# Optimization experiments

Measured on AMD Instinct MI355X. Metric: run time of the kernel, lower is better.

The kernel has to match this reference:

```python
import jax, jax.numpy as jnp
import numpy as np

# Model constants (match init_kwargs / input_specs)
D_MODEL = 64; N_HEADS = 4; D_HEAD = D_MODEL // N_HEADS
N_LAYERS = 2; D_FF = 256
N_GRAPHS = 256; NODES_PER = 64; N_NODES = N_GRAPHS * NODES_PER
DEG = 8; N_EDGES = N_NODES * DEG
VOCAB = 32; N_CLASS = 10


def setup_inputs() -> dict:
    rng = np.random.default_rng(0)
    # node labels
    x = jnp.asarray(rng.integers(0, VOCAB, N_NODES), dtype=jnp.int32)
    # sparse edge_index: each node receives DEG messages from random nodes in its own graph
    base = np.repeat(np.arange(N_NODES), DEG)
    nbr = (base // NODES_PER) * NODES_PER + rng.integers(0, NODES_PER, N_NODES * DEG)
    edge_index = jnp.asarray(np.stack([nbr, base]), dtype=jnp.int32)  # [2, E] (src, dst)
    # complete_edge_index: all (src, dst) pairs within each graph
    local = np.arange(NODES_PER); goff = np.arange(N_GRAPHS) * NODES_PER
    ii = np.repeat(local, NODES_PER); jj = np.tile(local, NODES_PER)
    c_src = (goff[:, None] + ii[None, :]).reshape(-1)
    c_dst = (goff[:, None] + jj[None, :]).reshape(-1)
    complete_edge_index = jnp.asarray(np.stack([c_src, c_dst]), dtype=jnp.int32)  # [2, 1048576]
    batch = jnp.asarray(np.repeat(np.arange(N_GRAPHS), NODES_PER), dtype=jnp.int32)

    key = jax.random.key(0)
    ks = jax.random.split(key, 12)
    s = 1.0 / np.sqrt(D_MODEL)
    W = lambda k, shape, sc: jax.random.normal(k, shape, jnp.float32) * sc
    return {
        'x': x, 'edge_index': edge_index, 'complete_edge_index': complete_edge_index, 'batch': batch,
        'emb': W(ks[0], (VOCAB, D_MODEL), 0.1),
        'Wg_self': W(ks[1], (N_LAYERS, D_MODEL, D_MODEL), s),
        'Wg_nbr': W(ks[2], (N_LAYERS, D_MODEL, D_MODEL), s),
        'Wq': W(ks[3], (N_LAYERS, D_MODEL, D_MODEL), s),
        'Wk': W(ks[4], (N_LAYERS, D_MODEL, D_MODEL), s),
        'Wv': W(ks[5], (N_LAYERS, D_MODEL, D_MODEL), s),
        'Wo': W(ks[6], (N_LAYERS, D_MODEL, D_MODEL), s),
        'bo': jnp.zeros((N_LAYERS, D_MODEL), jnp.float32),
        'ln1_g': jnp.ones((N_LAYERS, D_MODEL), jnp.float32),
        'ln1_b': jnp.zeros((N_LAYERS, D_MODEL), jnp.float32),
        'ff_W1': W(ks[7], (N_LAYERS, D_MODEL, D_FF), s),
        'ff_b1': jnp.zeros((N_LAYERS, D_FF), jnp.float32),
        'ff_W2': W(ks[8], (N_LAYERS, D_FF, D_MODEL), 1.0 / np.sqrt(D_FF)),
        'ff_b2': jnp.zeros((N_LAYERS, D_MODEL), jnp.float32),
        'ln2_g': jnp.ones((N_LAYERS, D_MODEL), jnp.float32),
        'ln2_b': jnp.zeros((N_LAYERS, D_MODEL), jnp.float32),
        'c_W1': W(ks[9], (D_MODEL, D_MODEL), s),
        'c_b1': jnp.zeros((D_MODEL,), jnp.float32),
        'c_W2': W(ks[10], (D_MODEL, N_CLASS), s),
        'c_b2': jnp.zeros((N_CLASS,), jnp.float32),
    }


def _layernorm(h, g, b):
    m = jnp.mean(h, -1, keepdims=True)
    v = jnp.var(h, -1, keepdims=True)
    return (h - m) * jax.lax.rsqrt(v + 1e-5) * g + b


def _forward(x, edge_index, complete_edge_index, batch, emb, Wg_self, Wg_nbr, Wq, Wk, Wv, Wo, bo,
             ln1_g, ln1_b, ff_W1, ff_b1, ff_W2, ff_b2, ln2_g, ln2_b, c_W1, c_b1, c_W2, c_b2):
    e_src, e_dst = edge_index[0], edge_index[1]
    c_src, c_dst = complete_edge_index[0], complete_edge_index[1]
    h = emb[x]  # [N, d] embedding lookup
    inv_sqrt = 1.0 / np.sqrt(D_HEAD)
    for i in range(N_LAYERS):
        # --- structure extractor: one GNN message-passing step over sparse edge_index ---
        agg = jax.ops.segment_sum((h @ Wg_nbr[i])[e_src], e_dst, num_segments=N_NODES)
        struct = h + jax.nn.relu(h @ Wg_self[i] + agg)
        # --- multi-head attention over complete_edge_index (full attention within graph) ---
        q = (struct @ Wq[i]).reshape(N_NODES, N_HEADS, D_HEAD)
        k = (struct @ Wk[i]).reshape(N_NODES, N_HEADS, D_HEAD)
        v = (h @ Wv[i]).reshape(N_NODES, N_HEADS, D_HEAD)
        scores = jnp.einsum('ehd,ehd->eh', q[c_dst], k[c_src]) * inv_sqrt  # [Ec, H]
        m = jax.ops.segment_max(scores, c_dst, num_segments=N_NODES)
        ex = jnp.exp(scores - m[c_dst])
        den = jax.ops.segment_sum(ex, c_dst, num_segments=N_NODES)
        alpha = ex / den[c_dst]  # segment softmax per destination node
        attn = jax.ops.segment_sum(alpha[:, :, None] * v[c_src], c_dst, num_segments=N_NODES)
        out = attn.reshape(N_NODES, D_MODEL) @ Wo[i] + bo[i]
        h = _layernorm(h + out, ln1_g[i], ln1_b[i])
        # --- feed-forward ---
        f = jax.nn.relu(h @ ff_W1[i] + ff_b1[i]) @ ff_W2[i] + ff_b2[i]
        h = _layernorm(h + f, ln2_g[i], ln2_b[i])
    # --- global mean pooling per graph + classifier ---
    counts = jax.ops.segment_sum(jnp.ones((N_NODES,), jnp.float32), batch, num_segments=N_GRAPHS)
    pooled = jax.ops.segment_sum(h, batch, num_segments=N_GRAPHS) / counts[:, None]
    return jax.nn.relu(pooled @ c_W1 + c_b1) @ c_W2 + c_b2  # [B, num_class]


def reference(x, edge_index, complete_edge_index, batch, emb, Wg_self, Wg_nbr, Wq, Wk, Wv, Wo, bo,
              ln1_g, ln1_b, ff_W1, ff_b1, ff_W2, ff_b2, ln2_g, ln2_b, c_W1, c_b1, c_W2, c_b2):
    return _forward(x, edge_index, complete_edge_index, batch, emb, Wg_self, Wg_nbr, Wq, Wk, Wv, Wo,
                    bo, ln1_g, ln1_b, ff_W1, ff_b1, ff_W2, ff_b2, ln2_g, ln2_b, c_W1, c_b1, c_W2, c_b2)
```

## Files before the change

kernel.cpp:

```cpp
#include <hip/hip_runtime.h>

#define NG 256
#define NPG 64
#define DM 64
#define DFF 256
#define NL 2
#define DEG 8
#define NCLS 10
#define S68 68
#define S132 132

#define HB0 0
#define AB0 4352
#define BB0 8704
#define QB0 13056
#define WS0 17408
#define F10 26112
#define POOLW 34560

typedef __attribute__((ext_vector_type(4))) float f32x4;
typedef __attribute__((ext_vector_type(4))) unsigned int u32x4;
typedef __attribute__((ext_vector_type(8))) __bf16 bf16x8;

__device__ __forceinline__ unsigned int packsplit(float x) {
    union { float f; unsigned int u; } a; a.f = x;
    const unsigned int t = a.u;
    const unsigned int hi = (t + 0x7FFFu + ((t >> 16) & 1u)) >> 16;
    union { unsigned int u; float f; } hf; hf.u = hi << 16;
    union { float f; unsigned int u; } b; b.f = x - hf.f;
    const unsigned int tl = b.u;
    const unsigned int lo = (tl + 0x7FFFu + ((tl >> 16) & 1u)) & 0xFFFF0000u;
    return hi | lo;
}
__device__ __forceinline__ float unpackf(unsigned int u) {
    union { unsigned int u; float f; } h, l;
    h.u = u << 16;
    l.u = u & 0xFFFF0000u;
    return h.f + l.f;
}

__device__ __forceinline__ void extract(u32x4 p0, u32x4 p1, u32x4& hi, u32x4& lo) {
    hi[0] = (p0[0] & 0xFFFFu) | (p0[1] << 16);
    hi[1] = (p0[2] & 0xFFFFu) | (p0[3] << 16);
    hi[2] = (p1[0] & 0xFFFFu) | (p1[1] << 16);
    hi[3] = (p1[2] & 0xFFFFu) | (p1[3] << 16);
    lo[0] = (p0[0] >> 16) | (p0[1] & 0xFFFF0000u);
    lo[1] = (p0[2] >> 16) | (p0[3] & 0xFFFF0000u);
    lo[2] = (p1[0] >> 16) | (p1[1] & 0xFFFF0000u);
    lo[3] = (p1[2] >> 16) | (p1[3] & 0xFFFF0000u);
}

__device__ __forceinline__ f32x4 mfma16(u32x4 a, u32x4 b, f32x4 c) {
    return __builtin_amdgcn_mfma_f32_16x16x32_bf16(
        __builtin_bit_cast(bf16x8, a), __builtin_bit_cast(bf16x8, b), c, 0, 0, 0);
}

__device__ __forceinline__ f32x4 mmchunk(const unsigned int* Ap, const unsigned int* Bp,
                                         f32x4 acc) {
    const u32x4 a0 = *(const u32x4*)Ap, a1 = *(const u32x4*)(Ap + 4);
    const u32x4 b0 = *(const u32x4*)Bp, b1 = *(const u32x4*)(Bp + 4);
    u32x4 ah, al, bh, bl;
    extract(a0, a1, ah, al);
    extract(b0, b1, bh, bl);
    acc = mfma16(ah, bh, acc);
    acc = mfma16(ah, bl, acc);
    acc = mfma16(al, bh, acc);
    return acc;
}

__device__ __forceinline__ f32x4 mm64(const unsigned int* Apk, const unsigned int* Wst,
                                      int wr, int wc, int l) {
    const int arow = (wr << 4) + (l & 15);
    const int bcol = (wc << 4) + (l & 15);
    const int kg = (l >> 4) << 3;
    f32x4 acc = {0.f, 0.f, 0.f, 0.f};
    acc = mmchunk(Apk + arow * S68 + kg,      Wst + bcol * S68 + kg,      acc);
    acc = mmchunk(Apk + arow * S68 + kg + 32, Wst + bcol * S68 + kg + 32, acc);
    return acc;
}

__device__ __forceinline__ void dwrite_f32(float* dst, f32x4 acc, int wr, int wc, int l) {
    const int col = (wc << 4) + (l & 15);
    const int r0 = (wr << 4) + ((l >> 4) << 2);
#pragma unroll
    for (int r = 0; r < 4; ++r) dst[(r0 + r) * S68 + col] = acc[r];
}

__device__ __forceinline__ void stageW(const float* W, unsigned int* ws, int tid) {
    const int k = tid >> 4, c4 = (tid & 15) << 2;
    const f32x4 w = *(const f32x4*)(W + k * DM + c4);
#pragma unroll
    for (int i = 0; i < 4; ++i) ws[(c4 + i) * S68 + k] = packsplit(w[i]);
}

__device__ __forceinline__ void layernorm(const float* src, unsigned int* dst,
                                          const float* gp, const float* bp, int n, int jg) {
    const f32x4 v = *(const f32x4*)(src + n * S68 + jg);
    float s1 = v[0] + v[1] + v[2] + v[3];
    float s2 = v[0]*v[0] + v[1]*v[1] + v[2]*v[2] + v[3]*v[3];
    s1 += __shfl_xor(s1, 1); s1 += __shfl_xor(s1, 2);
    s1 += __shfl_xor(s1, 4); s1 += __shfl_xor(s1, 8);
    s2 += __shfl_xor(s2, 1); s2 += __shfl_xor(s2, 2);
    s2 += __shfl_xor(s2, 4); s2 += __shfl_xor(s2, 8);
    const float mean = s1 * 0.015625f;
    const float var  = s2 * 0.015625f - mean * mean;
    const float rstd = rsqrtf(var + 1e-5f);
    const f32x4 gm = *(const f32x4*)(gp + jg);
    const f32x4 bt = *(const f32x4*)(bp + jg);
    u32x4 p;
#pragma unroll
    for (int j = 0; j < 4; ++j) p[j] = packsplit((v[j] - mean) * rstd * gm[j] + bt[j]);
    *(u32x4*)(dst + n * S68 + jg) = p;
}

extern "C" __global__ __launch_bounds__(1024)
void gt_main(const int* __restrict__ x, const int* __restrict__ e_src,
             const float* __restrict__ emb, const float* __restrict__ Wgs,
             const float* __restrict__ Wgn, const float* __restrict__ Wq,
             const float* __restrict__ Wk, const float* __restrict__ Wv,
             const float* __restrict__ Wo, const float* __restrict__ bo,
             const float* __restrict__ l1g, const float* __restrict__ l1b,
             const float* __restrict__ fW1, const float* __restrict__ fb1,
             const float* __restrict__ fW2, const float* __restrict__ fb2,
             const float* __restrict__ l2g, const float* __restrict__ l2b,
             const float* __restrict__ cW1, const float* __restrict__ cb1,
             const float* __restrict__ cW2, const float* __restrict__ cb2,
             float* __restrict__ out)
{
    __shared__ unsigned int pool[POOLW];
    unsigned int* Hb  = pool + HB0;
    unsigned int* Abu = pool + AB0;  float* Abf = (float*)Abu;
    unsigned int* Bbu = pool + BB0;  float* Bbf = (float*)Bbu;
    unsigned int* Qbu = pool + QB0;  float* Qbf = (float*)Qbu;
    unsigned int* WsA = pool + WS0;
    unsigned int* WsB = pool + WS0 + 4352;
    unsigned int* Ws  = pool + WS0;
    unsigned int* F1  = pool + F10;

    const int g = blockIdx.x, tid = threadIdx.x;
    const int w = tid >> 6, l = tid & 63;
    const int wr = w >> 2, wc = w & 3;
    const int n = tid >> 4, c = tid & 15, jg = c << 2;

    {
        const int lbl = x[g * NPG + n];
        const f32x4 e = *(const f32x4*)(emb + lbl * DM + jg);
        u32x4 p;
#pragma unroll
        for (int j = 0; j < 4; ++j) p[j] = packsplit(e[j]);
        *(u32x4*)(Hb + n * S68 + jg) = p;
    }
    __syncthreads();

    for (int lay = 0; lay < NL; ++lay) {
        const int o64 = lay * DM * DM;

        stageW(Wgn + o64, WsA, tid); __syncthreads();
        { f32x4 acc = mm64(Hb, WsA, wr, wc, l); dwrite_f32(Abf, acc, wr, wc, l); }
        __syncthreads();

        {
            f32x4 s = {0.f, 0.f, 0.f, 0.f};
            const int* es = e_src + (g * NPG + n) * DEG;
#pragma unroll
            for (int k = 0; k < DEG; ++k) {
                const int sr = es[k] - g * NPG;
                const f32x4 v4 = *(const f32x4*)(Abf + sr * S68 + jg);
                s[0] += v4[0]; s[1] += v4[1]; s[2] += v4[2]; s[3] += v4[3];
            }
            *(f32x4*)(Bbf + n * S68 + jg) = s;
        }
        __syncthreads();

        stageW(Wgs + o64, WsB, tid); __syncthreads();
        {
            f32x4 acc = mm64(Hb, WsB, wr, wc, l);
            const int col = (wc << 4) + (l & 15), r0 = (wr << 4) + ((l >> 4) << 2);
#pragma unroll
            for (int r = 0; r < 4; ++r) {
                const int row = r0 + r;
                const float v = fmaxf(acc[r] + Bbf[row * S68 + col], 0.f)
                                + unpackf(Hb[row * S68 + col]);
                Abu[row * S68 + col] = packsplit(v);
            }
        }
        __syncthreads();

        stageW(Wk + o64, WsA, tid); __syncthreads();
        { f32x4 acc = mm64(Abu, WsA, wr, wc, l); dwrite_f32(Bbf, acc, wr, wc, l); }
        __syncthreads();

        stageW(Wq + o64, WsB, tid); __syncthreads();
        { f32x4 acc = mm64(Abu, WsB, wr, wc, l); dwrite_f32(Qbf, acc, wr, wc, l); }
        __syncthreads();

        stageW(Wv + o64, WsA, tid); __syncthreads();
        { f32x4 acc = mm64(Hb, WsA, wr, wc, l); dwrite_f32(Abf, acc, wr, wc, l); }
        __syncthreads();

        {
            const f32x4 q4 = *(const f32x4*)(Qbf + n * S68 + jg);
            float o0 = 0.f, o1 = 0.f, o2 = 0.f, o3 = 0.f, m = -1e30f, ls = 0.f;
            for (int sr = 0; sr < NPG; ++sr) {
                const f32x4 k4 = *(const f32x4*)(Bbf + sr * S68 + jg);
                float s = q4[0]*k4[0] + q4[1]*k4[1] + q4[2]*k4[2] + q4[3]*k4[3];
                s += __shfl_xor(s, 1);
                s += __shfl_xor(s, 2);
                s *= 0.25f;
                const float mn  = fmaxf(m, s);
                const float fac = __expf(m - mn), wg = __expf(s - mn);
                ls = ls * fac + wg;
                const f32x4 v4 = *(const f32x4*)(Abf + sr * S68 + jg);
                o0 = o0 * fac + wg * v4[0]; o1 = o1 * fac + wg * v4[1];
                o2 = o2 * fac + wg * v4[2]; o3 = o3 * fac + wg * v4[3];
                m = mn;
            }
            const float il = 1.f / ls;
            u32x4 p;
            p[0] = packsplit(o0 * il); p[1] = packsplit(o1 * il);
            p[2] = packsplit(o2 * il); p[3] = packsplit(o3 * il);
            *(u32x4*)(Qbu + n * S68 + jg) = p;
        }
        __syncthreads();

        stageW(Wo + o64, WsB, tid); __syncthreads();
        {
            f32x4 acc = mm64(Qbu, WsB, wr, wc, l);
            const int col = (wc << 4) + (l & 15), r0 = (wr << 4) + ((l >> 4) << 2);
            const float bb = bo[lay * DM + col];
#pragma unroll
            for (int r = 0; r < 4; ++r) {
                const int row = r0 + r;
                Abf[row * S68 + col] = acc[r] + bb + unpackf(Hb[row * S68 + col]);
            }
        }
        __syncthreads();

        layernorm(Abf, Hb, l1g + lay * DM, l1b + lay * DM, n, jg);
        __syncthreads();

        f32x4 f2 = {0.f, 0.f, 0.f, 0.f};
        for (int hf = 0; hf < 2; ++hf) {
            {
                const int k = tid >> 4, c8 = (tid & 15) << 3;
                const float* src = fW1 + lay * DM * DFF + k * DFF + hf * 128 + c8;
                const f32x4 w0 = *(const f32x4*)src, w1 = *(const f32x4*)(src + 4);
#pragma unroll
                for (int i = 0; i < 4; ++i) Ws[(c8 + i) * S68 + k]     = packsplit(w0[i]);
#pragma unroll
                for (int i = 0; i < 4; ++i) Ws[(c8 + 4 + i) * S68 + k] = packsplit(w1[i]);
            }
            __syncthreads();
            {
                const int kg = (l >> 4) << 3, arow = (wr << 4) + (l & 15);
                const int r0 = (wr << 4) + ((l >> 4) << 2);
#pragma unroll
                for (int t = 0; t < 2; ++t) {
                    const int tc = ((wc + 4 * t) << 4) + (l & 15);
                    f32x4 acc = {0.f, 0.f, 0.f, 0.f};
                    acc = mmchunk(Hb + arow * S68 + kg,      Ws + tc * S68 + kg,      acc);
                    acc = mmchunk(Hb + arow * S68 + kg + 32, Ws + tc * S68 + kg + 32, acc);
                    const float b1 = fb1[lay * DFF + hf * 128 + tc];
#pragma unroll
                    for (int r = 0; r < 4; ++r)
                        F1[(r0 + r) * S132 + tc] = packsplit(fmaxf(acc[r] + b1, 0.f));
                }
            }
            __syncthreads();
            {
                const int kk = tid >> 3, c8 = (tid & 7) << 3;
                const float* src = fW2 + lay * DFF * DM + (hf * 128 + kk) * DM + c8;
                const f32x4 w0 = *(const f32x4*)src, w1 = *(const f32x4*)(src + 4);
#pragma unroll
                for (int i = 0; i < 4; ++i) Ws[(c8 + i) * S132 + kk]     = packsplit(w0[i]);
#pragma unroll
                for (int i = 0; i < 4; ++i) Ws[(c8 + 4 + i) * S132 + kk] = packsplit(w1[i]);
            }
            __syncthreads();
            {
                const int kg = (l >> 4) << 3;
                const int arow = (wr << 4) + (l & 15), bcol = (wc << 4) + (l & 15);
#pragma unroll
                for (int ch = 0; ch < 4; ++ch)
                    f2 = mmchunk(F1 + arow * S132 + kg + 32 * ch,
                                 Ws + bcol * S132 + kg + 32 * ch, f2);
            }
            __syncthreads();
        }
        {
            const int col = (wc << 4) + (l & 15), r0 = (wr << 4) + ((l >> 4) << 2);
            const float bb = fb2[lay * DM + col];
#pragma unroll
            for (int r = 0; r < 4; ++r) {
                const int row = r0 + r;
                Abf[row * S68 + col] = f2[r] + bb + unpackf(Hb[row * S68 + col]);
            }
        }
        __syncthreads();

        layernorm(Abf, Hb, l2g + lay * DM, l2b + lay * DM, n, jg);
        __syncthreads();
    }

    if (tid < DM) {
        float s = 0.f;
        for (int nn = 0; nn < NPG; ++nn) s += unpackf(Hb[nn * S68 + tid]);
        Abf[tid] = s * 0.015625f;
    }
    __syncthreads();
    if (tid < DM) {
        float acc = cb1[tid];
        for (int i = 0; i < DM; ++i) acc = fmaf(Abf[i], cW1[i * DM + tid], acc);
        Bbf[tid] = fmaxf(acc, 0.f);
    }
    __syncthreads();
    if (tid < NCLS) {
        float acc = cb2[tid];
        for (int i = 0; i < DM; ++i) acc = fmaf(Bbf[i], cW2[i * NCLS + tid], acc);
        out[g * NCLS + tid] = acc;
    }
}

extern "C" void kernel_launch(void* const* d_in, const int* in_sizes, int n_in,
                              void* d_out, int out_size, void* d_ws, size_t ws_size,
                              hipStream_t stream) {
    gt_main<<<dim3(NG), dim3(1024), 0, stream>>>(
        (const int*)d_in[0], (const int*)d_in[1],
        (const float*)d_in[4], (const float*)d_in[5], (const float*)d_in[6],
        (const float*)d_in[7], (const float*)d_in[8], (const float*)d_in[9],
        (const float*)d_in[10], (const float*)d_in[11],
        (const float*)d_in[12], (const float*)d_in[13],
        (const float*)d_in[14], (const float*)d_in[15],
        (const float*)d_in[16], (const float*)d_in[17],
        (const float*)d_in[18], (const float*)d_in[19],
        (const float*)d_in[20], (const float*)d_in[21],
        (const float*)d_in[22], (const float*)d_in[23],
        (float*)d_out);
}
```

Before: 78.23 us.

## Pre-split weights into global bf16 hi/lo layout once and read directly in MFMA

Adds a prep kernel that converts all layer weights into transposed packed bf16 hi/lo form in a global buffer (the workspace when it is large enough, otherwise a device global). The main kernel then reads MFMA B operands straight from global/L2 instead of having every block re-stage and re-split each weight into LDS with a barrier. This removes repeated per-block conversion work and many syncthreads, and shrinks LDS use. It also fuses the K and Q projections into one phase and folds the attention scale into q. The costs are an extra kernel launch and B-operand loads that now come from global memory rather than LDS.

```diff
diff --git a/kernel.cpp b/kernel.cpp
--- a/kernel.cpp
+++ b/kernel.cpp
@@ -14,9 +14,15 @@
 #define AB0 4352
 #define BB0 8704
 #define QB0 13056
-#define WS0 17408
-#define F10 26112
-#define POOLW 34560
+#define F10 17408
+#define POOLW 25856
+
+#define W64B 0
+#define FF1B 49152
+#define FF2B 81920
+#define WTOT 114688
+
+__device__ __align__(16) unsigned int g_w[WTOT];
 
 typedef __attribute__((ext_vector_type(4))) float f32x4;
 typedef __attribute__((ext_vector_type(4))) unsigned int u32x4;
@@ -68,14 +74,14 @@
     return acc;
 }
 
-__device__ __forceinline__ f32x4 mm64(const unsigned int* Apk, const unsigned int* Wst,
-                                      int wr, int wc, int l) {
+__device__ __forceinline__ f32x4 mm64g(const unsigned int* Apk, const unsigned int* Wg,
+                                       int wr, int wc, int l) {
     const int arow = (wr << 4) + (l & 15);
     const int bcol = (wc << 4) + (l & 15);
     const int kg = (l >> 4) << 3;
     f32x4 acc = {0.f, 0.f, 0.f, 0.f};
-    acc = mmchunk(Apk + arow * S68 + kg,      Wst + bcol * S68 + kg,      acc);
-    acc = mmchunk(Apk + arow * S68 + kg + 32, Wst + bcol * S68 + kg + 32, acc);
+    acc = mmchunk(Apk + arow * S68 + kg,      Wg + bcol * 64 + kg,      acc);
+    acc = mmchunk(Apk + arow * S68 + kg + 32, Wg + bcol * 64 + kg + 32, acc);
     return acc;
 }
 
@@ -84,13 +90,6 @@
     const int r0 = (wr << 4) + ((l >> 4) << 2);
 #pragma unroll
     for (int r = 0; r < 4; ++r) dst[(r0 + r) * S68 + col] = acc[r];
-}
-
-__device__ __forceinline__ void stageW(const float* W, unsigned int* ws, int tid) {
-    const int k = tid >> 4, c4 = (tid & 15) << 2;
-    const f32x4 w = *(const f32x4*)(W + k * DM + c4);
-#pragma unroll
-    for (int i = 0; i < 4; ++i) ws[(c4 + i) * S68 + k] = packsplit(w[i]);
 }
 
 __device__ __forceinline__ void layernorm(const float* src, unsigned int* dst,
@@ -113,34 +112,60 @@
     *(u32x4*)(dst + n * S68 + jg) = p;
 }
 
+extern "C" __global__ void gt_prep(const float* __restrict__ Wgn, const float* __restrict__ Wgs,
+                                   const float* __restrict__ Wk, const float* __restrict__ Wq,
+                                   const float* __restrict__ Wv, const float* __restrict__ Wo,
+                                   const float* __restrict__ fW1, const float* __restrict__ fW2,
+                                   unsigned int* wout)
+{
+    unsigned int* W = wout ? wout : g_w;
+    const int t = blockIdx.x * 256 + threadIdx.x;
+    float v; int d;
+    if (t < 49152) {
+        const int m = t >> 12, r = t & 4095, k = r >> 6, c = r & 63;
+        const int lay = m / 6, idx = m - lay * 6;
+        const float* s;
+        switch (idx) { case 0: s = Wgn; break; case 1: s = Wgs; break;
+                       case 2: s = Wk;  break; case 3: s = Wq;  break;
+                       case 4: s = Wv;  break; default: s = Wo; }
+        v = s[lay * 4096 + k * 64 + c];
+        d = (m << 12) + (c << 6) + k;
+    } else if (t < 81920) {
+        const int r = t - 49152, lay = r >> 14, q = r & 16383, k = q >> 8, c = q & 255;
+        v = fW1[lay * 16384 + k * 256 + c];
+        d = FF1B + lay * 16384 + (c << 6) + k;
+    } else {
+        const int r = t - 81920, lay = r >> 14, q = r & 16383, k = q >> 6, c = q & 63;
+        v = fW2[lay * 16384 + k * 64 + c];
+        d = FF2B + lay * 16384 + (c << 8) + k;
+    }
+    W[d] = packsplit(v);
+}
+
 extern "C" __global__ __launch_bounds__(1024)
 void gt_main(const int* __restrict__ x, const int* __restrict__ e_src,
-             const float* __restrict__ emb, const float* __restrict__ Wgs,
-             const float* __restrict__ Wgn, const float* __restrict__ Wq,
-             const float* __restrict__ Wk, const float* __restrict__ Wv,
-             const float* __restrict__ Wo, const float* __restrict__ bo,
+             const float* __restrict__ emb, const float* __restrict__ bo,
              const float* __restrict__ l1g, const float* __restrict__ l1b,
-             const float* __restrict__ fW1, const float* __restrict__ fb1,
-             const float* __restrict__ fW2, const float* __restrict__ fb2,
+             const float* __restrict__ fb1, const float* __restrict__ fb2,
              const float* __restrict__ l2g, const float* __restrict__ l2b,
              const float* __restrict__ cW1, const float* __restrict__ cb1,
              const float* __restrict__ cW2, const float* __restrict__ cb2,
+             const unsigned int* __restrict__ wext,
              float* __restrict__ out)
 {
-    __shared__ unsigned int pool[POOLW];
+    const unsigned int* gw = wext ? wext : g_w;
+
+    __shared__ __align__(16) unsigned int pool[POOLW];
     unsigned int* Hb  = pool + HB0;
     unsigned int* Abu = pool + AB0;  float* Abf = (float*)Abu;
     unsigned int* Bbu = pool + BB0;  float* Bbf = (float*)Bbu;
     unsigned int* Qbu = pool + QB0;  float* Qbf = (float*)Qbu;
-    unsigned int* WsA = pool + WS0;
-    unsigned int* WsB = pool + WS0 + 4352;
-    unsigned int* Ws  = pool + WS0;
     unsigned int* F1  = pool + F10;
 
     const int g = blockIdx.x, tid = threadIdx.x;
     const int w = tid >> 6, l = tid & 63;
     const int wr = w >> 2, wc = w & 3;
-    const int n = tid >> 4, c = tid & 15, jg = c << 2;
+    const int n = tid >> 4, jg = (tid & 15) << 2;
 
     {
         const int lbl = x[g * NPG + n];
@@ -153,10 +178,9 @@
     __syncthreads();
 
     for (int lay = 0; lay < NL; ++lay) {
-        const int o64 = lay * DM * DM;
-
-        stageW(Wgn + o64, WsA, tid); __syncthreads();
-        { f32x4 acc = mm64(Hb, WsA, wr, wc, l); dwrite_f32(Abf, acc, wr, wc, l); }
+        const int m0 = lay * 6;
+
+        { f32x4 acc = mm64g(Hb, gw + ((m0 + 0) << 12), wr, wc, l); dwrite_f32(Abf, acc, wr, wc, l); }
         __syncthreads();
 
         {
@@ -172,9 +196,8 @@
         }
         __syncthreads();
 
-        stageW(Wgs + o64, WsB, tid); __syncthreads();
-        {
-            f32x4 acc = mm64(Hb, WsB, wr, wc, l);
+        {
+            f32x4 acc = mm64g(Hb, gw + ((m0 + 1) << 12), wr, wc, l);
             const int col = (wc << 4) + (l & 15), r0 = (wr << 4) + ((l >> 4) << 2);
 #pragma unroll
             for (int r = 0; r < 4; ++r) {
@@ -186,27 +209,27 @@
         }
         __syncthreads();
 
-        stageW(Wk + o64, WsA, tid); __syncthreads();
-        { f32x4 acc = mm64(Abu, WsA, wr, wc, l); dwrite_f32(Bbf, acc, wr, wc, l); }
-        __syncthreads();
-
-        stageW(Wq + o64, WsB, tid); __syncthreads();
-        { f32x4 acc = mm64(Abu, WsB, wr, wc, l); dwrite_f32(Qbf, acc, wr, wc, l); }
-        __syncthreads();
-
-        stageW(Wv + o64, WsA, tid); __syncthreads();
-        { f32x4 acc = mm64(Hb, WsA, wr, wc, l); dwrite_f32(Abf, acc, wr, wc, l); }
-        __syncthreads();
-
-        {
-            const f32x4 q4 = *(const f32x4*)(Qbf + n * S68 + jg);
+        {
+            f32x4 acc = mm64g(Abu, gw + ((m0 + 2) << 12), wr, wc, l);
+            dwrite_f32(Bbf, acc, wr, wc, l);
+            f32x4 acq = mm64g(Abu, gw + ((m0 + 3) << 12), wr, wc, l);
+            dwrite_f32(Qbf, acq, wr, wc, l);
+        }
+        __syncthreads();
+        { f32x4 acc = mm64g(Hb, gw + ((m0 + 4) << 12), wr, wc, l); dwrite_f32(Abf, acc, wr, wc, l); }
+        __syncthreads();
+
+        {
+            const f32x4 qr = *(const f32x4*)(Qbf + n * S68 + jg);
+            const float q0 = qr[0] * 0.25f, q1 = qr[1] * 0.25f;
+            const float q2 = qr[2] * 0.25f, q3 = qr[3] * 0.25f;
             float o0 = 0.f, o1 = 0.f, o2 = 0.f, o3 = 0.f, m = -1e30f, ls = 0.f;
+#pragma unroll 4
             for (int sr = 0; sr < NPG; ++sr) {
                 const f32x4 k4 = *(const f32x4*)(Bbf + sr * S68 + jg);
-                float s = q4[0]*k4[0] + q4[1]*k4[1] + q4[2]*k4[2] + q4[3]*k4[3];
+                float s = q0*k4[0] + q1*k4[1] + q2*k4[2] + q3*k4[3];
                 s += __shfl_xor(s, 1);
                 s += __shfl_xor(s, 2);
-                s *= 0.25f;
                 const float mn  = fmaxf(m, s);
                 const float fac = __expf(m - mn), wg = __expf(s - mn);
                 ls = ls * fac + wg;
@@ -223,9 +246,8 @@
         }
         __syncthreads();
 
-        stageW(Wo + o64, WsB, tid); __syncthreads();
-        {
-            f32x4 acc = mm64(Qbu, WsB, wr, wc, l);
+        {
+            f32x4 acc = mm64g(Qbu, gw + ((m0 + 5) << 12), wr, wc, l);
             const int col = (wc << 4) + (l & 15), r0 = (wr << 4) + ((l >> 4) << 2);
             const float bb = bo[lay * DM + col];
 #pragma unroll
@@ -242,48 +264,29 @@
         f32x4 f2 = {0.f, 0.f, 0.f, 0.f};
         for (int hf = 0; hf < 2; ++hf) {
             {
-                const int k = tid >> 4, c8 = (tid & 15) << 3;
-                const float* src = fW1 + lay * DM * DFF + k * DFF + hf * 128 + c8;
-                const f32x4 w0 = *(const f32x4*)src, w1 = *(const f32x4*)(src + 4);
-#pragma unroll
-                for (int i = 0; i < 4; ++i) Ws[(c8 + i) * S68 + k]     = packsplit(w0[i]);
-#pragma unroll
-                for (int i = 0; i < 4; ++i) Ws[(c8 + 4 + i) * S68 + k] = packsplit(w1[i]);
-            }
-            __syncthreads();
-            {
                 const int kg = (l >> 4) << 3, arow = (wr << 4) + (l & 15);
                 const int r0 = (wr << 4) + ((l >> 4) << 2);
 #pragma unroll
                 for (int t = 0; t < 2; ++t) {
                     const int tc = ((wc + 4 * t) << 4) + (l & 15);
+                    const unsigned int* Bp = gw + FF1B + lay * 16384 + ((hf * 128 + tc) << 6) + kg;
                     f32x4 acc = {0.f, 0.f, 0.f, 0.f};
-                    acc = mmchunk(Hb + arow * S68 + kg,      Ws + tc * S68 + kg,      acc);
-                    acc = mmchunk(Hb + arow * S68 + kg + 32, Ws + tc * S68 + kg + 32, acc);
+                    acc = mmchunk(Hb + arow * S68 + kg,      Bp,      acc);
+                    acc = mmchunk(Hb + arow * S68 + kg + 32, Bp + 32, acc);
                     const float b1 = fb1[lay * DFF + hf * 128 + tc];
 #pragma unroll
                     for (int r = 0; r < 4; ++r)
                         F1[(r0 + r) * S132 + tc] = packsplit(fmaxf(acc[r] + b1, 0.f));
                 }
-            }
-            __syncthreads();
-            {
-                const int kk = tid >> 3, c8 = (tid & 7) << 3;
-                const float* src = fW2 + lay * DFF * DM + (hf * 128 + kk) * DM + c8;
-                const f32x4 w0 = *(const f32x4*)src, w1 = *(const f32x4*)(src + 4);
-#pragma unroll
-                for (int i = 0; i < 4; ++i) Ws[(c8 + i) * S132 + kk]     = packsplit(w0[i]);
-#pragma unroll
-                for (int i = 0; i < 4; ++i) Ws[(c8 + 4 + i) * S132 + kk] = packsplit(w1[i]);
             }
             __syncthreads();
             {
                 const int kg = (l >> 4) << 3;
                 const int arow = (wr << 4) + (l & 15), bcol = (wc << 4) + (l & 15);
+                const unsigned int* Bp = gw + FF2B + lay * 16384 + (bcol << 8) + hf * 128 + kg;
 #pragma unroll
                 for (int ch = 0; ch < 4; ++ch)
-                    f2 = mmchunk(F1 + arow * S132 + kg + 32 * ch,
-                                 Ws + bcol * S132 + kg + 32 * ch, f2);
+                    f2 = mmchunk(F1 + arow * S132 + kg + 32 * ch, Bp + 32 * ch, f2);
             }
             __syncthreads();
         }
@@ -324,16 +327,22 @@
 extern "C" void kernel_launch(void* const* d_in, const int* in_sizes, int n_in,
                               void* d_out, int out_size, void* d_ws, size_t ws_size,
                               hipStream_t stream) {
+    unsigned int* wbuf =
+        (d_ws != nullptr && ws_size >= (size_t)WTOT * 4) ? (unsigned int*)d_ws : nullptr;
+    gt_prep<<<dim3(448), dim3(256), 0, stream>>>(
+        (const float*)d_in[6], (const float*)d_in[5],
+        (const float*)d_in[8], (const float*)d_in[7],
+        (const float*)d_in[9], (const float*)d_in[10],
+        (const float*)d_in[14], (const float*)d_in[16],
+        wbuf);
     gt_main<<<dim3(NG), dim3(1024), 0, stream>>>(
         (const int*)d_in[0], (const int*)d_in[1],
-        (const float*)d_in[4], (const float*)d_in[5], (const float*)d_in[6],
-        (const float*)d_in[7], (const float*)d_in[8], (const float*)d_in[9],
-        (const float*)d_in[10], (const float*)d_in[11],
+        (const float*)d_in[4], (const float*)d_in[11],
         (const float*)d_in[12], (const float*)d_in[13],
-        (const float*)d_in[14], (const float*)d_in[15],
-        (const float*)d_in[16], (const float*)d_in[17],
+        (const float*)d_in[15], (const float*)d_in[17],
         (const float*)d_in[18], (const float*)d_in[19],
         (const float*)d_in[20], (const float*)d_in[21],
         (const float*)d_in[22], (const float*)d_in[23],
+        wbuf,
         (float*)d_out);
 }
```

After: 95.71 us. 1.22x slower.
